# Optimization experiments

Hardware: AMD Instinct MI355X
Metric: run time of the kernel (lower is better)

The kernel has to match this reference:

```python
import jax, jax.numpy as jnp
import numpy as np

B, T, C, H = 4, 2048, 768, 12
D = C // H  # head dim = 64


def setup_inputs() -> dict:
    key = jax.random.key(0)
    k1, k2, k3, k4 = jax.random.split(key, 4)
    x = jax.random.normal(k1, (B, T, C), dtype=jnp.float32)
    attn_mask = jnp.ones((B, T), dtype=jnp.float32)
    layer_lambda = jax.random.uniform(k2, (H,), dtype=jnp.float32)
    W_attn = jax.random.normal(k3, (C, 3 * C), dtype=jnp.float32) * (1.0 / np.sqrt(C))
    W_proj = jax.random.normal(k4, (C, C), dtype=jnp.float32) * (1.0 / np.sqrt(C))
    return {"x": x, "attn_mask": attn_mask, "layer_lambda": layer_lambda,
            "W_attn": W_attn, "W_proj": W_proj}


def reference(x, attn_mask, layer_lambda, W_attn, W_proj):
    Bx, Tx, Cx = x.shape
    qkv = x @ W_attn                      # (B, T, 3C)
    q, k, v = jnp.split(qkv, 3, axis=2)
    # (B, H, T, D)
    q = q.reshape(Bx, Tx, H, D).transpose(0, 2, 1, 3)
    k = k.reshape(Bx, Tx, H, D).transpose(0, 2, 1, 3)
    v = v.reshape(Bx, Tx, H, D).transpose(0, 2, 1, 3)

    att = jnp.einsum('bhqd,bhkd->bhqk', q, k) / jnp.sqrt(jnp.float32(D))

    # log-scale bias: scale row q of scores by (1 + lambda_h * log(q+1))
    log_pos = jnp.log(jnp.arange(Tx, dtype=jnp.float32) + 1.0)  # (T,)
    scale = 1.0 + layer_lambda[None, :, None, None] * log_pos[None, None, :, None]
    att = att * scale

    causal = jnp.tril(jnp.ones((Tx, Tx), dtype=jnp.float32))            # (T, T)
    mask = causal[None, None, :, :] * attn_mask[:, None, None, :]       # (B,1,T,T)

    # relu_attention path: relu, mask, normalize by row sum
    att = jax.nn.relu(att) * mask
    att_weights = att / (att.sum(axis=-1, keepdims=True) + 1e-9)

    out = jnp.einsum('bhqk,bhkd->bhqd', att_weights, v)  # (B, H, T, D)
    out = out.transpose(0, 2, 1, 3).reshape(Bx, Tx, Cx)
    return out @ W_proj
```

## Files before the change

kernel.cpp:

```cpp
#include <hip/hip_runtime.h>
#include <cstddef>
#include <cstdint>

#define Bn 4
#define Tn 2048
#define Cn 768
#define Hn 12

typedef __attribute__((ext_vector_type(8))) short short8v;
typedef __attribute__((ext_vector_type(4))) float f32x4;
typedef unsigned short ushort_t;

struct us4 { unsigned short x, y, z, w; };

__device__ inline unsigned short f2bf(float f) {
  union { float f; unsigned u; } v; v.f = f;
  unsigned r = v.u + 0x7FFFu + ((v.u >> 16) & 1u);
  return (unsigned short)(r >> 16);
}
__device__ inline float bf2f(unsigned short u) {
  union { unsigned u; float f; } v; v.u = ((unsigned)u) << 16;
  return v.f;
}
__device__ inline unsigned cvt_pk_bf16(float lo, float hi) {
  unsigned r;
  asm("v_cvt_pk_bf16_f32 %0, %1, %2" : "=v"(r) : "v"(lo), "v"(hi));
  return r;
}

#define GLOAD_LDS16(gp, lp)                                                        \
  __builtin_amdgcn_global_load_lds(                                                \
      (const __attribute__((address_space(1))) void*)(gp),                         \
      (__attribute__((address_space(3))) void*)(lp), 16, 0, 0)

__global__ __launch_bounds__(256) void conv_x_split(const float* __restrict__ in,
                                                    ushort_t* __restrict__ hi,
                                                    ushort_t* __restrict__ lo, int n4) {
  int i = blockIdx.x * 256 + threadIdx.x;
  if (i >= n4) return;
  float4 v = reinterpret_cast<const float4*>(in)[i];
  us4 h;
  h.x = f2bf(v.x); h.y = f2bf(v.y); h.z = f2bf(v.z); h.w = f2bf(v.w);
  reinterpret_cast<us4*>(hi)[i] = h;
  const int row = (i << 2) / Cn;
  if ((row & (Tn - 1)) < 256) {
    us4 l;
    l.x = f2bf(v.x - bf2f(h.x)); l.y = f2bf(v.y - bf2f(h.y));
    l.z = f2bf(v.z - bf2f(h.z)); l.w = f2bf(v.w - bf2f(h.w));
    reinterpret_cast<us4*>(lo)[i] = l;
  }
}

__global__ __launch_bounds__(256) void conv_w_both(
    const float* __restrict__ Wa, ushort_t* __restrict__ WaTh,
    ushort_t* __restrict__ WaTl, const float* __restrict__ Wp,
    ushort_t* __restrict__ WpT) {
  __shared__ float t[64][65];
  const bool split = (blockIdx.x < 36);
  const float* W = split ? Wa : Wp;
  ushort_t* WTh  = split ? WaTh : WpT;
  const int cols = split ? 3 * Cn : Cn;
  const int c0   = (split ? blockIdx.x : (blockIdx.x - 36)) * 64;
  const int r0   = blockIdx.y * 64;
  const int rows = Cn;
  const int tid = threadIdx.x;
  const int c4 = (tid & 15) << 2;
  #pragma unroll
  for (int rr = 0; rr < 4; ++rr) {
    int r = rr * 16 + (tid >> 4);
    float4 v = *reinterpret_cast<const float4*>(&W[(size_t)(r0 + r) * cols + c0 + c4]);
    t[r][c4] = v.x; t[r][c4 + 1] = v.y; t[r][c4 + 2] = v.z; t[r][c4 + 3] = v.w;
  }
  __syncthreads();
  const int r4 = (tid & 15) << 2;
  #pragma unroll
  for (int cc = 0; cc < 4; ++cc) {
    int c = cc * 16 + (tid >> 4);
    float v0 = t[r4][c], v1 = t[r4 + 1][c], v2 = t[r4 + 2][c], v3 = t[r4 + 3][c];
    us4 h;
    h.x = f2bf(v0); h.y = f2bf(v1); h.z = f2bf(v2); h.w = f2bf(v3);
    *reinterpret_cast<us4*>(&WTh[(size_t)(c0 + c) * rows + r0 + r4]) = h;
    if (split) {
      us4 l;
      l.x = f2bf(v0 - bf2f(h.x)); l.y = f2bf(v1 - bf2f(h.y));
      l.z = f2bf(v2 - bf2f(h.z)); l.w = f2bf(v3 - bf2f(h.w));
      *reinterpret_cast<us4*>(&WaTl[(size_t)(c0 + c) * rows + r0 + r4]) = l;
    }
  }
}

template <int COMP, int MODE, int SLICE, int WLO, int MT>
__global__ __launch_bounds__(256) void gemm_bf16(
    const ushort_t* __restrict__ Ah, const ushort_t* __restrict__ Al,
    const ushort_t* __restrict__ Bh, const ushort_t* __restrict__ Bl,
    int M, int N, int K, int bn_off, int nbx, float* __restrict__ C,
    const float* __restrict__ lambda,
    ushort_t* __restrict__ qhp, ushort_t* __restrict__ qlp,
    ushort_t* __restrict__ khp, ushort_t* __restrict__ klp,
    ushort_t* __restrict__ vtp) {
  constexpr int MFRAG = MT / 32;
  __shared__ ushort_t As[2][MT * 64];
  __shared__ ushort_t Bs[2][128 * 64];

  const int tid = threadIdx.x;
  const int w = tid >> 6;
  const int lane = tid & 63;
  const int lcol = lane & 15;
  const int g = lane >> 4;
  const int id = (blockIdx.x & 7) * (gridDim.x >> 3) + (blockIdx.x >> 3);
  const int bxi = id % nbx;
  const int byi = id / nbx;
  const int bm = SLICE ? ((byi >> 1) * Tn + (byi & 1) * 128) : (byi * MT);
  const int bn = bxi * 128 + bn_off;
  const int wr = (w >> 1) * (MT / 2);
  const int wc = (w & 1) * 64;
  const int srow = tid >> 3;
  const int sslot = tid & 7;

  f32x4 acc[MFRAG][4];
  #pragma unroll
  for (int m = 0; m < MFRAG; ++m)
    #pragma unroll
    for (int n = 0; n < 4; ++n)
      acc[m][n] = (f32x4){0.f, 0.f, 0.f, 0.f};

  auto STAGE_A = [&](int k0, int buf, const ushort_t* A) {
    #pragma unroll
    for (int i = 0; i < MT / 32; ++i) {
      const int row = i * 32 + srow;
      const int kslot = sslot ^ (row & 7);
      GLOAD_LDS16(A + (size_t)(bm + row) * K + k0 + kslot * 8,
                  (char*)As[buf] + (size_t)(i * 256 + tid) * 16);
    }
  };
  auto STAGE_B = [&](int k0, int buf, const ushort_t* B) {
    #pragma unroll
    for (int i = 0; i < 4; ++i) {
      const int row = i * 32 + srow;
      const int kslot = sslot ^ (row & 7);
      GLOAD_LDS16(B + (size_t)(bn + row) * K + k0 + kslot * 8,
                  (char*)Bs[buf] + (size_t)(i * 256 + tid) * 16);
    }
  };

  const int nt = K >> 6;
  if constexpr (COMP == 0) {
    STAGE_A(0, 0, Ah); STAGE_B(0, 0, Bh);
    __syncthreads();
    for (int t = 0; t < nt; ++t) {
      const int cur = t & 1;
      if (t + 1 < nt) { STAGE_A((t + 1) << 6, cur ^ 1, Ah); STAGE_B((t + 1) << 6, cur ^ 1, Bh); }
      #pragma unroll
      for (int kk = 0; kk < 2; ++kk) {
        short8v a0[MFRAG], b0[4];
        #pragma unroll
        for (int m = 0; m < MFRAG; ++m) {
          int row = wr + m * 16 + lcol;
          a0[m] = *reinterpret_cast<const short8v*>(
              (const char*)As[cur] + row * 128 + (((kk * 4 + g) ^ (row & 7)) << 4));
        }
        #pragma unroll
        for (int n = 0; n < 4; ++n) {
          int row = wc + n * 16 + lcol;
          b0[n] = *reinterpret_cast<const short8v*>(
              (const char*)Bs[cur] + row * 128 + (((kk * 4 + g) ^ (row & 7)) << 4));
        }
        #pragma unroll
        for (int m = 0; m < MFRAG; ++m)
          #pragma unroll
          for (int n = 0; n < 4; ++n)
            acc[m][n] = __builtin_amdgcn_mfma_f32_16x16x32_bf16(a0[m], b0[n], acc[m][n], 0, 0, 0);
      }
      __syncthreads();
    }
  } else {
    for (int t = 0; t < nt; ++t) {
      const int k0 = t << 6;
      __syncthreads();
      STAGE_A(k0, 0, Ah); STAGE_B(k0, 0, Bh);
      STAGE_A(k0, 1, Al); STAGE_B(k0, 1, Bl);
      __syncthreads();
      #pragma unroll
      for (int kk = 0; kk < 2; ++kk) {
        short8v a0[MFRAG], b0[4], a1[MFRAG], b1[4];
        #pragma unroll
        for (int m = 0; m < MFRAG; ++m) {
          int row = wr + m * 16 + lcol;
          int off = row * 128 + (((kk * 4 + g) ^ (row & 7)) << 4);
          a0[m] = *reinterpret_cast<const short8v*>((const char*)As[0] + off);
          a1[m] = *reinterpret_cast<const short8v*>((const char*)As[1] + off);
        }
        #pragma unroll
        for (int n = 0; n < 4; ++n) {
          int row = wc + n * 16 + lcol;
          int off = row * 128 + (((kk * 4 + g) ^ (row & 7)) << 4);
          b0[n] = *reinterpret_cast<const short8v*>((const char*)Bs[0] + off);
          b1[n] = *reinterpret_cast<const short8v*>((const char*)Bs[1] + off);
        }
        #pragma unroll
        for (int m = 0; m < MFRAG; ++m)
          #pragma unroll
          for (int n = 0; n < 4; ++n) {
            acc[m][n] = __builtin_amdgcn_mfma_f32_16x16x32_bf16(a0[m], b0[n], acc[m][n], 0, 0, 0);
            acc[m][n] = __builtin_amdgcn_mfma_f32_16x16x32_bf16(a0[m], b1[n], acc[m][n], 0, 0, 0);
            acc[m][n] = __builtin_amdgcn_mfma_f32_16x16x32_bf16(a1[m], b0[n], acc[m][n], 0, 0, 0);
          }
      }
    }
  }

  if (MODE == 0) {
    #pragma unroll
    for (int m = 0; m < MFRAG; ++m) {
      const int rowm = bm + wr + m * 16 + g * 4;
      #pragma unroll
      for (int n = 0; n < 4; ++n) {
        const int col = bn + wc + n * 16 + lcol;
        #pragma unroll
        for (int j = 0; j < 4; ++j)
          C[(size_t)(rowm + j) * N + col] = acc[m][n][j];
      }
    }
  } else {
    const int seg = bn / Cn;
    const int nloc_base = bn - seg * Cn + wc;
    #pragma unroll
    for (int m = 0; m < MFRAG; ++m) {
      const int mg = bm + wr + m * 16 + g * 4;
      const int bidx = mg >> 11;
      const int tbase = mg & (Tn - 1);
      float lgt[4];
      if (seg == 0) {
        #pragma unroll
        for (int j = 0; j < 4; ++j) lgt[j] = logf((float)(tbase + j) + 1.0f);
      }
      const bool wqk = (WLO || tbase >= 256);
      #pragma unroll
      for (int n = 0; n < 4; ++n) {
        const int nloc = nloc_base + n * 16 + lcol;
        const int h = nloc >> 6;
        const int d = nloc & 63;
        const size_t bhh = (size_t)(bidx * Hn + h);
        if (seg == 0) {
          if (wqk) {
            const float lam = lambda[h];
            #pragma unroll
            for (int j = 0; j < 4; ++j) {
              float val = acc[m][n][j] * (0.125f * (1.0f + lam * lgt[j]));
              unsigned short hi = f2bf(val);
              size_t idx = (bhh * Tn + tbase + j) * 64 + d;
              qhp[idx] = hi;
              if (WLO) qlp[idx] = f2bf(val - bf2f(hi));
            }
          }
        } else if (seg == 1) {
          if (wqk) {
            #pragma unroll
            for (int j = 0; j < 4; ++j) {
              float val = acc[m][n][j];
              unsigned short hi = f2bf(val);
              size_t idx = (bhh * Tn + tbase + j) * 64 + d;
              khp[idx] = hi;
              if (WLO) klp[idx] = f2bf(val - bf2f(hi));
            }
          }
        } else {
          const int kt_ = tbase >> 6;
          const int tl_ = tbase & 63;
          us4 pv;
          pv.x = f2bf(acc[m][n][0]); pv.y = f2bf(acc[m][n][1]);
          pv.z = f2bf(acc[m][n][2]); pv.w = f2bf(acc[m][n][3]);
          *reinterpret_cast<us4*>(
              &vtp[(((bhh * 32 + kt_) * 64 + d) << 6) + tl_]) = pv;
        }
      }
    }
  }
}

__global__ __launch_bounds__(256) void attn_mfma(
    const ushort_t* __restrict__ qh, const ushort_t* __restrict__ ql,
    const ushort_t* __restrict__ kh, const ushort_t* __restrict__ kl,
    const ushort_t* __restrict__ vt, const float* __restrict__ attn_mask,
    ushort_t* __restrict__ ao) {
  const int xcd = blockIdx.x & 7;
  const int idx = blockIdx.x >> 3;
  const int bh  = xcd * 6 + (idx % 6);
  const int pr  = idx / 6;
  const int b = bh / Hn, h = bh % Hn;
  const int tid = threadIdx.x;
  const int w = tid >> 6, lane = tid & 63, lcol = lane & 15, g = lane >> 4;

  __shared__ ushort_t Kh_lds[2][64 * 64];
  __shared__ ushort_t V_lds[2][64 * 64];
  __shared__ ushort_t P_lds[4][16 * 64];

  for (int segq = 0; segq < 2; ++segq) {
    const int qt = segq ? (31 - pr) : pr;
    const bool compq = (qt <= 3);

    const size_t qoff0 = ((size_t)bh * Tn + qt * 64 + w * 16 + lcol) * 64;
    short8v qfh0 = *reinterpret_cast<const short8v*>(qh + qoff0 + g * 8);
    short8v qfh1 = *reinterpret_cast<const short8v*>(qh + qoff0 + 32 + g * 8);

    f32x4 o[4];
    #pragma unroll
    for (int dt = 0; dt < 4; ++dt) o[dt] = (f32x4){0.f, 0.f, 0.f, 0.f};
    float dsum = 0.f;

    auto STAGE = [&](int kt, int d) {
      const ushort_t* ks = kh + ((size_t)bh * Tn + kt * 64) * 64;
      const ushort_t* vs = vt + ((size_t)bh * 32 + kt) * 64 * 64;
      #pragma unroll
      for (int it = 0; it < 2; ++it) {
        const int s = it * 256 + tid;
        const int row = s >> 3, sslot = s & 7;
        const int swz = (sslot ^ (row & 7)) * 8;
        GLOAD_LDS16(ks + row * 64 + swz, (char*)Kh_lds[d] + (size_t)s * 16);
        GLOAD_LDS16(vs + row * 64 + swz, (char*)V_lds[d] + (size_t)s * 16);
      }
    };
    auto STAGE_KL = [&](int kt) {
      const ushort_t* ls = kl + ((size_t)bh * Tn + kt * 64) * 64;
      #pragma unroll
      for (int it = 0; it < 2; ++it) {
        const int s = it * 256 + tid;
        const int row = s >> 3, sslot = s & 7;
        const int swz = (sslot ^ (row & 7)) * 8;
        GLOAD_LDS16(ls + row * 64 + swz, (char*)Kh_lds[1] + (size_t)s * 16);
      }
    };

    auto COMPUTE = [&](int kt, int d, bool cq, bool ck) {
      float4 mv4[4];
      #pragma unroll
      for (int c = 0; c < 4; ++c)
        mv4[c] = *reinterpret_cast<const float4*>(
            &attn_mask[b * Tn + kt * 64 + c * 16 + g * 4]);
      const bool diag = (kt == qt);
      const int qr = qt * 64 + w * 16 + lcol;
      short8v qfl0, qfl1;
      if (cq) {
        qfl0 = *reinterpret_cast<const short8v*>(ql + qoff0 + g * 8);
        qfl1 = *reinterpret_cast<const short8v*>(ql + qoff0 + 32 + g * 8);
      }
      char* pb = (char*)P_lds[w];
      const int pswz = (lcol & 7) << 4;
      #pragma unroll
      for (int c = 0; c < 4; ++c) {
        const int row = c * 16 + lcol;
        const int roff = row * 128;
        const int s0 = (g ^ (row & 7)) << 4;
        const int s1 = ((4 + g) ^ (row & 7)) << 4;
        short8v kf0 = *reinterpret_cast<const short8v*>((const char*)Kh_lds[d] + roff + s0);
        short8v kf1 = *reinterpret_cast<const short8v*>((const char*)Kh_lds[d] + roff + s1);
        f32x4 s = (f32x4){0.f, 0.f, 0.f, 0.f};
        __builtin_amdgcn_s_setprio(1);
        s = __builtin_amdgcn_mfma_f32_16x16x32_bf16(kf0, qfh0, s, 0, 0, 0);
        s = __builtin_amdgcn_mfma_f32_16x16x32_bf16(kf1, qfh1, s, 0, 0, 0);
        if (cq) {
          s = __builtin_amdgcn_mfma_f32_16x16x32_bf16(kf0, qfl0, s, 0, 0, 0);
          s = __builtin_amdgcn_mfma_f32_16x16x32_bf16(kf1, qfl1, s, 0, 0, 0);
        }
        if (ck) {
          short8v kl0 = *reinterpret_cast<const short8v*>((const char*)Kh_lds[1] + roff + s0);
          short8v kl1 = *reinterpret_cast<const short8v*>((const char*)Kh_lds[1] + roff + s1);
          s = __builtin_amdgcn_mfma_f32_16x16x32_bf16(kl0, qfh0, s, 0, 0, 0);
          s = __builtin_amdgcn_mfma_f32_16x16x32_bf16(kl1, qfh1, s, 0, 0, 0);
        }
        __builtin_amdgcn_s_setprio(0);
        const float* mvp = &mv4[c].x;
        float sv[4];
        #pragma unroll
        for (int r = 0; r < 4; ++r) {
          float v = fmaxf(s[r], 0.f) * mvp[r];
          if (diag) {
            const int kr = kt * 64 + c * 16 + g * 4 + r;
            v = (kr <= qr) ? v : 0.f;
          }
          sv[r] = v;
        }
        const unsigned p01 = cvt_pk_bf16(sv[0], sv[1]);
        const unsigned p23 = cvt_pk_bf16(sv[2], sv[3]);
        *reinterpret_cast<uint2*>(pb + lcol * 128 + ((c * 32 + g * 8) ^ pswz)) =
            make_uint2(p01, p23);
        dsum += (sv[0] + sv[1]) + (sv[2] + sv[3]);
      }
      short8v pf0 = *reinterpret_cast<const short8v*>(pb + lcol * 128 + ((g * 16) ^ pswz));
      short8v pf1 = *reinterpret_cast<const short8v*>(pb + lcol * 128 + ((64 + g * 16) ^ pswz));
      __builtin_amdgcn_s_setprio(1);
      #pragma unroll
      for (int dt = 0; dt < 4; ++dt) {
        const int vrow = dt * 16 + lcol;
        const int vro = vrow * 128;
        short8v vf0 = *reinterpret_cast<const short8v*>(
            (const char*)V_lds[d] + vro + ((g ^ (vrow & 7)) << 4));
        short8v vf1 = *reinterpret_cast<const short8v*>(
            (const char*)V_lds[d] + vro + (((4 + g) ^ (vrow & 7)) << 4));
        o[dt] = __builtin_amdgcn_mfma_f32_16x16x32_bf16(pf0, vf0, o[dt], 0, 0, 0);
        o[dt] = __builtin_amdgcn_mfma_f32_16x16x32_bf16(pf1, vf1, o[dt], 0, 0, 0);
      }
      __builtin_amdgcn_s_setprio(0);
    };

    if (qt <= 1) {
      for (int kt = 0; kt <= qt; ++kt) {
        STAGE(kt, 0);
        STAGE_KL(kt);
        __syncthreads();
        COMPUTE(kt, 0, true, true);
        __syncthreads();
      }
    } else {
      const int ntiles = qt + 1;
      STAGE(0, 0);
      __syncthreads();
      for (int kt = 0; kt < ntiles; ++kt) {
        const int d = kt & 1;
        if (kt + 1 < ntiles) STAGE(kt + 1, d ^ 1);
        COMPUTE(kt, d, compq, false);
        __syncthreads();
      }
    }

    float dtot = dsum;
    dtot += __shfl_xor(dtot, 16);
    dtot += __shfl_xor(dtot, 32);
    const float invq = 1.0f / (dtot + 1e-9f);
    float invs[4];
    #pragma unroll
    for (int r = 0; r < 4; ++r) invs[r] = __shfl(invq, g * 4 + r);

    ushort_t* ob = ao + ((size_t)b * Tn + qt * 64 + w * 16) * Cn + h * 64;
    #pragma unroll
    for (int dt = 0; dt < 4; ++dt)
      #pragma unroll
      for (int r = 0; r < 4; ++r)
        ob[(size_t)(g * 4 + r) * Cn + dt * 16 + lcol] = f2bf(o[dt][r] * invs[r]);
  }
}

extern "C" void kernel_launch(void* const* d_in, const int* in_sizes, int n_in,
                              void* d_out, int out_size, void* d_ws, size_t ws_size,
                              hipStream_t stream) {
  const float* x         = (const float*)d_in[0];
  const float* attn_mask = (const float*)d_in[1];
  const float* lambda    = (const float*)d_in[2];
  const float* W_attn    = (const float*)d_in[3];
  const float* W_proj    = (const float*)d_in[4];
  float* out = (float*)d_out;

  const size_t nBTC = (size_t)Bn * Tn * Cn;
  const size_t nW1  = (size_t)Cn * 3 * Cn;
  const size_t nW2  = (size_t)Cn * Cn;
  ushort_t* xh  = (ushort_t*)d_ws;
  ushort_t* xl  = xh + nBTC;
  ushort_t* WhT = xl + nBTC;
  ushort_t* WlT = WhT + nW1;
  ushort_t* WpT = WlT + nW1;
  ushort_t* qh  = WpT + nW2;
  ushort_t* ql  = qh + nBTC;
  ushort_t* kh  = ql + nBTC;
  ushort_t* kl  = kh + nBTC;
  ushort_t* vt  = kl + nBTC;
  ushort_t* ao  = xh;

  dim3 blk(256);

  conv_x_split<<<dim3((unsigned)(nBTC / 4 / 256)), blk, 0, stream>>>(
      x, xh, xl, (int)(nBTC / 4));
  conv_w_both<<<dim3(48, 12), blk, 0, stream>>>(W_attn, WhT, WlT, W_proj, WpT);

  gemm_bf16<0, 1, 0, 0, 128><<<dim3(1152), blk, 0, stream>>>(
      xh, nullptr, WhT, nullptr, Bn * Tn, 3 * Cn, Cn, 0, 18, nullptr, lambda,
      qh, ql, kh, kl, vt);
  gemm_bf16<1, 1, 1, 1, 128><<<dim3(96), blk, 0, stream>>>(
      xh, xl, WhT, WlT, Bn * Tn, 3 * Cn, Cn, 0, 12, nullptr, lambda,
      qh, ql, kh, kl, vt);

  attn_mfma<<<dim3(768), blk, 0, stream>>>(
      qh, ql, kh, kl, vt, attn_mask, ao);

  gemm_bf16<0, 0, 0, 0, 64><<<dim3(768), blk, 0, stream>>>(
      ao, nullptr, WpT, nullptr, Bn * Tn, Cn, Cn, 0, 6, out, nullptr,
      nullptr, nullptr, nullptr, nullptr, nullptr);
}
```

Measured before the change: 160.4 us.

## Merge prep kernels and fuse QKV GEMM passes into single launches

New measurement: 157.0 us. 2.2% less time.

```diff
diff --git a/kernel.cpp b/kernel.cpp
--- a/kernel.cpp
+++ b/kernel.cpp
@@ -33,37 +33,39 @@
       (const __attribute__((address_space(1))) void*)(gp),                         \
       (__attribute__((address_space(3))) void*)(lp), 16, 0, 0)
 
-__global__ __launch_bounds__(256) void conv_x_split(const float* __restrict__ in,
-                                                    ushort_t* __restrict__ hi,
-                                                    ushort_t* __restrict__ lo, int n4) {
-  int i = blockIdx.x * 256 + threadIdx.x;
-  if (i >= n4) return;
-  float4 v = reinterpret_cast<const float4*>(in)[i];
-  us4 h;
-  h.x = f2bf(v.x); h.y = f2bf(v.y); h.z = f2bf(v.z); h.w = f2bf(v.w);
-  reinterpret_cast<us4*>(hi)[i] = h;
-  const int row = (i << 2) / Cn;
-  if ((row & (Tn - 1)) < 256) {
-    us4 l;
-    l.x = f2bf(v.x - bf2f(h.x)); l.y = f2bf(v.y - bf2f(h.y));
-    l.z = f2bf(v.z - bf2f(h.z)); l.w = f2bf(v.w - bf2f(h.w));
-    reinterpret_cast<us4*>(lo)[i] = l;
-  }
-}
-
-__global__ __launch_bounds__(256) void conv_w_both(
+__global__ __launch_bounds__(256) void prep_all(
+    const float* __restrict__ x, ushort_t* __restrict__ xh, ushort_t* __restrict__ xl,
     const float* __restrict__ Wa, ushort_t* __restrict__ WaTh,
     ushort_t* __restrict__ WaTl, const float* __restrict__ Wp,
     ushort_t* __restrict__ WpT) {
   __shared__ float t[64][65];
-  const bool split = (blockIdx.x < 36);
+  const int blk = blockIdx.x;
+  const int tid = threadIdx.x;
+  if (blk < 6144) {
+    const int i = blk * 256 + tid;
+    float4 v = reinterpret_cast<const float4*>(x)[i];
+    us4 h;
+    h.x = f2bf(v.x); h.y = f2bf(v.y); h.z = f2bf(v.z); h.w = f2bf(v.w);
+    reinterpret_cast<us4*>(xh)[i] = h;
+    const int row = (i << 2) / Cn;
+    if ((row & (Tn - 1)) < 256) {
+      us4 l;
+      l.x = f2bf(v.x - bf2f(h.x)); l.y = f2bf(v.y - bf2f(h.y));
+      l.z = f2bf(v.z - bf2f(h.z)); l.w = f2bf(v.w - bf2f(h.w));
+      reinterpret_cast<us4*>(xl)[i] = l;
+    }
+    return;
+  }
+  const int id2 = blk - 6144;
+  const int cx  = id2 % 48;
+  const int ry  = id2 / 48;
+  const bool split = (cx < 36);
   const float* W = split ? Wa : Wp;
   ushort_t* WTh  = split ? WaTh : WpT;
   const int cols = split ? 3 * Cn : Cn;
-  const int c0   = (split ? blockIdx.x : (blockIdx.x - 36)) * 64;
-  const int r0   = blockIdx.y * 64;
+  const int c0   = (split ? cx : (cx - 36)) * 64;
+  const int r0   = ry * 64;
   const int rows = Cn;
-  const int tid = threadIdx.x;
   const int c4 = (tid & 15) << 2;
   #pragma unroll
   for (int rr = 0; rr < 4; ++rr) {
@@ -89,17 +91,15 @@
   }
 }
 
-template <int COMP, int MODE, int SLICE, int WLO, int MT>
-__global__ __launch_bounds__(256) void gemm_bf16(
+__global__ __launch_bounds__(256) void gemm_qkv_fused(
     const ushort_t* __restrict__ Ah, const ushort_t* __restrict__ Al,
     const ushort_t* __restrict__ Bh, const ushort_t* __restrict__ Bl,
-    int M, int N, int K, int bn_off, int nbx, float* __restrict__ C,
     const float* __restrict__ lambda,
     ushort_t* __restrict__ qhp, ushort_t* __restrict__ qlp,
     ushort_t* __restrict__ khp, ushort_t* __restrict__ klp,
     ushort_t* __restrict__ vtp) {
-  constexpr int MFRAG = MT / 32;
-  __shared__ ushort_t As[2][MT * 64];
+  constexpr int K = Cn, N = 3 * Cn;
+  __shared__ ushort_t As[2][128 * 64];
   __shared__ ushort_t Bs[2][128 * 64];
 
   const int tid = threadIdx.x;
@@ -108,25 +108,32 @@
   const int lcol = lane & 15;
   const int g = lane >> 4;
   const int id = (blockIdx.x & 7) * (gridDim.x >> 3) + (blockIdx.x >> 3);
-  const int bxi = id % nbx;
-  const int byi = id / nbx;
-  const int bm = SLICE ? ((byi >> 1) * Tn + (byi & 1) * 128) : (byi * MT);
-  const int bn = bxi * 128 + bn_off;
-  const int wr = (w >> 1) * (MT / 2);
+  const bool comp = (id >= 1152);
+  int bm, bn;
+  if (!comp) {
+    bm = (id / 18) * 128;
+    bn = (id % 18) * 128;
+  } else {
+    const int id2 = id - 1152;
+    const int byi = id2 / 12;
+    bm = (byi >> 1) * Tn + (byi & 1) * 128;
+    bn = (id2 % 12) * 128;
+  }
+  const int wr = (w >> 1) * 64;
   const int wc = (w & 1) * 64;
   const int srow = tid >> 3;
   const int sslot = tid & 7;
 
-  f32x4 acc[MFRAG][4];
+  f32x4 acc[4][4];
   #pragma unroll
-  for (int m = 0; m < MFRAG; ++m)
+  for (int m = 0; m < 4; ++m)
     #pragma unroll
     for (int n = 0; n < 4; ++n)
       acc[m][n] = (f32x4){0.f, 0.f, 0.f, 0.f};
 
   auto STAGE_A = [&](int k0, int buf, const ushort_t* A) {
     #pragma unroll
-    for (int i = 0; i < MT / 32; ++i) {
+    for (int i = 0; i < 4; ++i) {
       const int row = i * 32 + srow;
       const int kslot = sslot ^ (row & 7);
       GLOAD_LDS16(A + (size_t)(bm + row) * K + k0 + kslot * 8,
@@ -144,7 +151,7 @@
   };
 
   const int nt = K >> 6;
-  if constexpr (COMP == 0) {
+  if (!comp) {
     STAGE_A(0, 0, Ah); STAGE_B(0, 0, Bh);
     __syncthreads();
     for (int t = 0; t < nt; ++t) {
@@ -152,9 +159,9 @@
       if (t + 1 < nt) { STAGE_A((t + 1) << 6, cur ^ 1, Ah); STAGE_B((t + 1) << 6, cur ^ 1, Bh); }
       #pragma unroll
       for (int kk = 0; kk < 2; ++kk) {
-        short8v a0[MFRAG], b0[4];
-        #pragma unroll
-        for (int m = 0; m < MFRAG; ++m) {
+        short8v a0[4], b0[4];
+        #pragma unroll
+        for (int m = 0; m < 4; ++m) {
           int row = wr + m * 16 + lcol;
           a0[m] = *reinterpret_cast<const short8v*>(
               (const char*)As[cur] + row * 128 + (((kk * 4 + g) ^ (row & 7)) << 4));
@@ -166,7 +173,7 @@
               (const char*)Bs[cur] + row * 128 + (((kk * 4 + g) ^ (row & 7)) << 4));
         }
         #pragma unroll
-        for (int m = 0; m < MFRAG; ++m)
+        for (int m = 0; m < 4; ++m)
           #pragma unroll
           for (int n = 0; n < 4; ++n)
             acc[m][n] = __builtin_amdgcn_mfma_f32_16x16x32_bf16(a0[m], b0[n], acc[m][n], 0, 0, 0);
@@ -182,9 +189,9 @@
       __syncthreads();
       #pragma unroll
       for (int kk = 0; kk < 2; ++kk) {
-        short8v a0[MFRAG], b0[4], a1[MFRAG], b1[4];
-        #pragma unroll
-        for (int m = 0; m < MFRAG; ++m) {
+        short8v a0[4], b0[4], a1[4], b1[4];
+        #pragma unroll
+        for (int m = 0; m < 4; ++m) {
           int row = wr + m * 16 + lcol;
           int off = row * 128 + (((kk * 4 + g) ^ (row & 7)) << 4);
           a0[m] = *reinterpret_cast<const short8v*>((const char*)As[0] + off);
@@ -198,7 +205,7 @@
           b1[n] = *reinterpret_cast<const short8v*>((const char*)Bs[1] + off);
         }
         #pragma unroll
-        for (int m = 0; m < MFRAG; ++m)
+        for (int m = 0; m < 4; ++m)
           #pragma unroll
           for (int n = 0; n < 4; ++n) {
             acc[m][n] = __builtin_amdgcn_mfma_f32_16x16x32_bf16(a0[m], b0[n], acc[m][n], 0, 0, 0);
@@ -209,71 +216,146 @@
     }
   }
 
-  if (MODE == 0) {
-    #pragma unroll
-    for (int m = 0; m < MFRAG; ++m) {
-      const int rowm = bm + wr + m * 16 + g * 4;
+  const int seg = bn / Cn;
+  const int nloc_base = bn - seg * Cn + wc;
+  #pragma unroll
+  for (int m = 0; m < 4; ++m) {
+    const int mg = bm + wr + m * 16 + g * 4;
+    const int bidx = mg >> 11;
+    const int tbase = mg & (Tn - 1);
+    float lgt[4];
+    if (seg == 0) {
+      #pragma unroll
+      for (int j = 0; j < 4; ++j) lgt[j] = logf((float)(tbase + j) + 1.0f);
+    }
+    const bool wqk = comp ? true : (tbase >= 256);
+    #pragma unroll
+    for (int n = 0; n < 4; ++n) {
+      const int nloc = nloc_base + n * 16 + lcol;
+      const int h = nloc >> 6;
+      const int d = nloc & 63;
+      const size_t bhh = (size_t)(bidx * Hn + h);
+      if (seg == 0) {
+        if (wqk) {
+          const float lam = lambda[h];
+          #pragma unroll
+          for (int j = 0; j < 4; ++j) {
+            float val = acc[m][n][j] * (0.125f * (1.0f + lam * lgt[j]));
+            unsigned short hi = f2bf(val);
+            size_t idx = (bhh * Tn + tbase + j) * 64 + d;
+            qhp[idx] = hi;
+            if (comp) qlp[idx] = f2bf(val - bf2f(hi));
+          }
+        }
+      } else if (seg == 1) {
+        if (wqk) {
+          #pragma unroll
+          for (int j = 0; j < 4; ++j) {
+            float val = acc[m][n][j];
+            unsigned short hi = f2bf(val);
+            size_t idx = (bhh * Tn + tbase + j) * 64 + d;
+            khp[idx] = hi;
+            if (comp) klp[idx] = f2bf(val - bf2f(hi));
+          }
+        }
+      } else {
+        const int kt_ = tbase >> 6;
+        const int tl_ = tbase & 63;
+        us4 pv;
+        pv.x = f2bf(acc[m][n][0]); pv.y = f2bf(acc[m][n][1]);
+        pv.z = f2bf(acc[m][n][2]); pv.w = f2bf(acc[m][n][3]);
+        *reinterpret_cast<us4*>(
+            &vtp[(((bhh * 32 + kt_) * 64 + d) << 6) + tl_]) = pv;
+      }
+    }
+  }
+}
+
+__global__ __launch_bounds__(256) void gemm_proj(
+    const ushort_t* __restrict__ Ah, const ushort_t* __restrict__ Bh,
+    float* __restrict__ C) {
+  constexpr int K = Cn, N = Cn, MT = 64;
+  __shared__ ushort_t As[2][MT * 64];
+  __shared__ ushort_t Bs[2][128 * 64];
+
+  const int tid = threadIdx.x;
+  const int w = tid >> 6;
+  const int lane = tid & 63;
+  const int lcol = lane & 15;
+  const int g = lane >> 4;
+  const int id = (blockIdx.x & 7) * (gridDim.x >> 3) + (blockIdx.x >> 3);
+  const int bm = (id / 6) * MT;
+  const int bn = (id % 6) * 128;
+  const int wr = (w >> 1) * 32;
+  const int wc = (w & 1) * 64;
+  const int srow = tid >> 3;
+  const int sslot = tid & 7;
+
+  f32x4 acc[2][4];
+  #pragma unroll
+  for (int m = 0; m < 2; ++m)
+    #pragma unroll
+    for (int n = 0; n < 4; ++n)
+      acc[m][n] = (f32x4){0.f, 0.f, 0.f, 0.f};
+
+  auto STAGE_A = [&](int k0, int buf) {
+    #pragma unroll
+    for (int i = 0; i < 2; ++i) {
+      const int row = i * 32 + srow;
+      const int kslot = sslot ^ (row & 7);
+      GLOAD_LDS16(Ah + (size_t)(bm + row) * K + k0 + kslot * 8,
+                  (char*)As[buf] + (size_t)(i * 256 + tid) * 16);
+    }
+  };
+  auto STAGE_B = [&](int k0, int buf) {
+    #pragma unroll
+    for (int i = 0; i < 4; ++i) {
+      const int row = i * 32 + srow;
+      const int kslot = sslot ^ (row & 7);
+      GLOAD_LDS16(Bh + (size_t)(bn + row) * K + k0 + kslot * 8,
+                  (char*)Bs[buf] + (size_t)(i * 256 + tid) * 16);
+    }
+  };
+
+  const int nt = K >> 6;
+  STAGE_A(0, 0); STAGE_B(0, 0);
+  __syncthreads();
+  for (int t = 0; t < nt; ++t) {
+    const int cur = t & 1;
+    if (t + 1 < nt) { STAGE_A((t + 1) << 6, cur ^ 1); STAGE_B((t + 1) << 6, cur ^ 1); }
+    #pragma unroll
+    for (int kk = 0; kk < 2; ++kk) {
+      short8v a0[2], b0[4];
+      #pragma unroll
+      for (int m = 0; m < 2; ++m) {
+        int row = wr + m * 16 + lcol;
+        a0[m] = *reinterpret_cast<const short8v*>(
+            (const char*)As[cur] + row * 128 + (((kk * 4 + g) ^ (row & 7)) << 4));
+      }
       #pragma unroll
       for (int n = 0; n < 4; ++n) {
-        const int col = bn + wc + n * 16 + lcol;
-        #pragma unroll
-        for (int j = 0; j < 4; ++j)
-          C[(size_t)(rowm + j) * N + col] = acc[m][n][j];
-      }
-    }
-  } else {
-    const int seg = bn / Cn;
-    const int nloc_base = bn - seg * Cn + wc;
-    #pragma unroll
-    for (int m = 0; m < MFRAG; ++m) {
-      const int mg = bm + wr + m * 16 + g * 4;
-      const int bidx = mg >> 11;
-      const int tbase = mg & (Tn - 1);
-      float lgt[4];
-      if (seg == 0) {
-        #pragma unroll
-        for (int j = 0; j < 4; ++j) lgt[j] = logf((float)(tbase + j) + 1.0f);
-      }
-      const bool wqk = (WLO || tbase >= 256);
-      #pragma unroll
-      for (int n = 0; n < 4; ++n) {
-        const int nloc = nloc_base + n * 16 + lcol;
-        const int h = nloc >> 6;
-        const int d = nloc & 63;
-        const size_t bhh = (size_t)(bidx * Hn + h);
-        if (seg == 0) {
-          if (wqk) {
-            const float lam = lambda[h];
-            #pragma unroll
-            for (int j = 0; j < 4; ++j) {
-              float val = acc[m][n][j] * (0.125f * (1.0f + lam * lgt[j]));
-              unsigned short hi = f2bf(val);
-              size_t idx = (bhh * Tn + tbase + j) * 64 + d;
-              qhp[idx] = hi;
-              if (WLO) qlp[idx] = f2bf(val - bf2f(hi));
-            }
-          }
-        } else if (seg == 1) {
-          if (wqk) {
-            #pragma unroll
-            for (int j = 0; j < 4; ++j) {
-              float val = acc[m][n][j];
-              unsigned short hi = f2bf(val);
-              size_t idx = (bhh * Tn + tbase + j) * 64 + d;
-              khp[idx] = hi;
-              if (WLO) klp[idx] = f2bf(val - bf2f(hi));
-            }
-          }
-        } else {
-          const int kt_ = tbase >> 6;
-          const int tl_ = tbase & 63;
-          us4 pv;
-          pv.x = f2bf(acc[m][n][0]); pv.y = f2bf(acc[m][n][1]);
-          pv.z = f2bf(acc[m][n][2]); pv.w = f2bf(acc[m][n][3]);
-          *reinterpret_cast<us4*>(
-              &vtp[(((bhh * 32 + kt_) * 64 + d) << 6) + tl_]) = pv;
-        }
-      }
+        int row = wc + n * 16 + lcol;
+        b0[n] = *reinterpret_cast<const short8v*>(
+            (const char*)Bs[cur] + row * 128 + (((kk * 4 + g) ^ (row & 7)) << 4));
+      }
+      #pragma unroll
+      for (int m = 0; m < 2; ++m)
+        #pragma unroll
+        for (int n = 0; n < 4; ++n)
+          acc[m][n] = __builtin_amdgcn_mfma_f32_16x16x32_bf16(a0[m], b0[n], acc[m][n], 0, 0, 0);
+    }
+    __syncthreads();
+  }
+
+  #pragma unroll
+  for (int m = 0; m < 2; ++m) {
+    const int rowm = bm + wr + m * 16 + g * 4;
+    #pragma unroll
+    for (int n = 0; n < 4; ++n) {
+      const int col = bn + wc + n * 16 + lcol;
+      #pragma unroll
+      for (int j = 0; j < 4; ++j)
+        C[(size_t)(rowm + j) * N + col] = acc[m][n][j];
     }
   }
 }
@@ -371,14 +453,16 @@
         __builtin_amdgcn_s_setprio(0);
         const float* mvp = &mv4[c].x;
         float sv[4];
-        #pragma unroll
-        for (int r = 0; r < 4; ++r) {
-          float v = fmaxf(s[r], 0.f) * mvp[r];
-          if (diag) {
+        if (diag) {
+          #pragma unroll
+          for (int r = 0; r < 4; ++r) {
+            float v = fmaxf(s[r], 0.f) * mvp[r];
             const int kr = kt * 64 + c * 16 + g * 4 + r;
-            v = (kr <= qr) ? v : 0.f;
+            sv[r] = (kr <= qr) ? v : 0.f;
           }
-          sv[r] = v;
+        } else {
+          #pragma unroll
+          for (int r = 0; r < 4; ++r) sv[r] = fmaxf(s[r], 0.f) * mvp[r];
         }
         const unsigned p01 = cvt_pk_bf16(sv[0], sv[1]);
         const unsigned p23 = cvt_pk_bf16(sv[2], sv[3]);
@@ -467,21 +551,14 @@
 
   dim3 blk(256);
 
-  conv_x_split<<<dim3((unsigned)(nBTC / 4 / 256)), blk, 0, stream>>>(
-      x, xh, xl, (int)(nBTC / 4));
-  conv_w_both<<<dim3(48, 12), blk, 0, stream>>>(W_attn, WhT, WlT, W_proj, WpT);
-
-  gemm_bf16<0, 1, 0, 0, 128><<<dim3(1152), blk, 0, stream>>>(
-      xh, nullptr, WhT, nullptr, Bn * Tn, 3 * Cn, Cn, 0, 18, nullptr, lambda,
-      qh, ql, kh, kl, vt);
-  gemm_bf16<1, 1, 1, 1, 128><<<dim3(96), blk, 0, stream>>>(
-      xh, xl, WhT, WlT, Bn * Tn, 3 * Cn, Cn, 0, 12, nullptr, lambda,
-      qh, ql, kh, kl, vt);
+  prep_all<<<dim3(6720), blk, 0, stream>>>(
+      x, xh, xl, W_attn, WhT, WlT, W_proj, WpT);
+
+  gemm_qkv_fused<<<dim3(1248), blk, 0, stream>>>(
+      xh, xl, WhT, WlT, lambda, qh, ql, kh, kl, vt);
 
   attn_mfma<<<dim3(768), blk, 0, stream>>>(
       qh, ql, kh, kl, vt, attn_mask, ao);
 
-  gemm_bf16<0, 0, 0, 0, 64><<<dim3(768), blk, 0, stream>>>(
-      ao, nullptr, WpT, nullptr, Bn * Tn, Cn, Cn, 0, 6, out, nullptr,
-      nullptr, nullptr, nullptr, nullptr, nullptr);
-}
+  gemm_proj<<<dim3(768), blk, 0, stream>>>(ao, WpT, out);
+}
```
